# Kernel tuning notes

Measured on AMD Instinct MI355X. Metric: run time of the kernel, lower is better.

The kernel has to match this reference:

```python
import jax, jax.numpy as jnp
import numpy as np
from jax import lax

E, D, I, K = 8, 1024, 2048, 2
B, S = 4, 1024


def setup_inputs() -> dict:
    key = jax.random.key(0)
    k1, k2, k3, k4, k5 = jax.random.split(key, 5)
    x = jax.random.normal(k1, (B, S, D), dtype=jnp.float32)
    routing_weights = jax.random.uniform(k2, (B, S, K), dtype=jnp.float32)
    selected_experts = jax.random.randint(k3, (B, S, K), 0, E).astype(jnp.int64)
    w1 = 0.02 * jax.random.normal(k4, (E, D, I), dtype=jnp.float32)
    w2 = 0.02 * jax.random.normal(k5, (E, I, D), dtype=jnp.float32)
    return {"x": x, "routing_weights": routing_weights,
            "selected_experts": selected_experts, "w1": w1, "w2": w2}


def reference(x, routing_weights, selected_experts, w1, w2):
    shape = x.shape
    d = shape[-1]
    xf = x.reshape(-1, d)                       # [T, D]
    rw = routing_weights.reshape(xf.shape[0], -1)   # [T, K]
    se = selected_experts.reshape(xf.shape[0], -1)  # [T, K]
    n_experts = w1.shape[0]

    def body(acc, inputs):
        e, w1e, w2e = inputs
        # per-token combine weight for expert e (rw assumed >= 0; zero weight == not routed)
        wt = jnp.sum(jnp.where(se == e, rw, 0.0), axis=-1)  # [T]
        h = jax.nn.silu(xf @ w1e)                # [T, I]
        out = h @ w2e                            # [T, D]
        return acc + out * wt[:, None], None

    acc0 = jnp.zeros_like(xf)
    acc, _ = lax.scan(body, acc0, (jnp.arange(n_experts), w1, w2))
    return acc.reshape(shape)
```

## Files before the change

kernel.cpp:

```cpp
#include <hip/hip_runtime.h>
#include <stdint.h>

#define E_EXPERTS 8
#define D_DIM 1024
#define I_DIM 2048
#define T_TOKENS 4096
#define NSLOTS 8192
#define TILE 128
#define MAXPAD (NSLOTS + E_EXPERTS * TILE)
#define TPX 9

#define XCVT_BLOCKS 2048
#define PREP_GRID (1 + XCVT_BLOCKS + 4096)

typedef __attribute__((ext_vector_type(8))) short bf16x8;
typedef __attribute__((ext_vector_type(4))) float f32x4;

__device__ __forceinline__ unsigned short f2b(float f) {
  union { float f; uint32_t u; } v; v.f = f;
  uint32_t r = v.u + 0x7FFFu + ((v.u >> 16) & 1u);
  return (unsigned short)(r >> 16);
}
__device__ __forceinline__ float b2f(unsigned short u) {
  union { uint32_t u; float f; } v; v.u = ((uint32_t)u) << 16; return v.f;
}

__device__ __forceinline__ void async16(const unsigned short* g, unsigned short* l) {
  __builtin_amdgcn_global_load_lds(
      (const __attribute__((address_space(1))) void*)g,
      (__attribute__((address_space(3))) void*)l, 16, 0, 0);
}

__global__ __launch_bounds__(256) void prep_k(
    const float* __restrict__ x, const float* __restrict__ w1, const float* __restrict__ w2,
    const int* __restrict__ se,
    unsigned short* __restrict__ xb, unsigned short* __restrict__ w1t,
    unsigned short* __restrict__ w2t,
    int* __restrict__ ntiles, int* __restrict__ desc,
    int* __restrict__ tok, int* __restrict__ slot_of) {
  int b = blockIdx.x;
  int tid = threadIdx.x;

  if (b == 0) {
    __shared__ int scnt[E_EXPERTS], sbase[E_EXPERTS + 1], scur[E_EXPERTS];
    if (tid < E_EXPERTS) scnt[tid] = 0;
    __syncthreads();
    for (int s = tid; s < NSLOTS; s += 256) atomicAdd(&scnt[se[s]], 1);
    __syncthreads();
    if (tid == 0) {
      int acc = 0, nt = 0;
      for (int e = 0; e < E_EXPERTS; e++) {
        int n = scnt[e];
        sbase[e] = acc;
        scur[e] = acc;
        int pad = (n + TILE - 1) & ~(TILE - 1);
        for (int m = 0; m * TILE < pad; m++) { desc[2 * nt] = e; desc[2 * nt + 1] = acc + m * TILE; nt++; }
        acc += pad;
      }
      sbase[E_EXPERTS] = acc;
      *ntiles = nt;
    }
    __syncthreads();
    for (int e = 0; e < E_EXPERTS; e++) {
      int s0 = sbase[e] + scnt[e], s1 = sbase[e + 1];
      for (int s = s0 + tid; s < s1; s += 256) tok[s] = 0;
    }
    for (int s = tid; s < NSLOTS; s += 256) {
      int e = se[s];
      int pos = atomicAdd(&scur[e], 1);
      tok[pos] = s >> 1;
      slot_of[s] = pos;
    }
    return;
  }

  int bb = b - 1;

  if (bb < XCVT_BLOCKS) {
    size_t i = ((size_t)bb * 256 + tid) * 8;
    float4 v0 = *(const float4*)(x + i);
    float4 v1 = *(const float4*)(x + i + 4);
    ushort4 o0, o1;
    o0.x = f2b(v0.x); o0.y = f2b(v0.y); o0.z = f2b(v0.z); o0.w = f2b(v0.w);
    o1.x = f2b(v1.x); o1.y = f2b(v1.y); o1.z = f2b(v1.z); o1.w = f2b(v1.w);
    *(ushort4*)(xb + i) = o0;
    *(ushort4*)(xb + i + 4) = o1;
    return;
  }

  __shared__ float ts[64 * 129];
  int wb = bb - XCVT_BLOCKS;
  int mat = wb >> 11;
  int sub = wb & 2047;
  int e = sub >> 8, rem = sub & 255;
  const float* src; unsigned short* dst; int C, k0, n0;
  if (mat == 0) {
    int nt = rem >> 4, kt = rem & 15;
    C = I_DIM; k0 = kt * 64; n0 = nt * 128;
    src = w1 + (size_t)e * D_DIM * I_DIM;
    dst = w1t + ((size_t)((e * 16 + nt) * 16 + kt)) * 8192;
  } else {
    int nt = rem >> 5, kt = rem & 31;
    C = D_DIM; k0 = kt * 64; n0 = nt * 128;
    src = w2 + (size_t)e * D_DIM * I_DIM;
    dst = w2t + ((size_t)((e * 8 + nt) * 32 + kt)) * 8192;
  }

  int lrow = tid & 7, c4 = (tid >> 3) * 4;
#pragma unroll
  for (int i = 0; i < 8; i++) {
    int row = i * 8 + lrow;
    float4 v = *(const float4*)(src + (size_t)(k0 + row) * C + n0 + c4);
    float* d = ts + row * 129 + c4;
    d[0] = v.x; d[1] = v.y; d[2] = v.z; d[3] = v.w;
  }
  __syncthreads();
#pragma unroll
  for (int j = 0; j < 4; j++) {
    int q = j * 256 + tid;
    int rr = q >> 3, cc8 = q & 7;
    int c = cc8 ^ (rr & 7);
    bf16x8 o;
#pragma unroll
    for (int t = 0; t < 8; t++)
      o[t] = (short)f2b(ts[(c * 8 + t) * 129 + rr]);
    *(bf16x8*)(dst + (size_t)q * 8) = o;
  }
}

template <int KLEN, int KFULL, int NDIM, int PHASE>
__global__ __launch_bounds__(256) void moe_gemm_k(
    const unsigned short* __restrict__ Amat, const unsigned short* __restrict__ Bt,
    const int* __restrict__ desc, const int* __restrict__ ntiles_p,
    const int* __restrict__ tok, unsigned short* __restrict__ Hout) {
  int id = blockIdx.x;
  int xcd = id & 7, r = id >> 3;
  int ti = xcd * TPX + r % TPX;
  int q = r / TPX;
  int nb, kh;
  if (PHASE == 1) { nb = q; kh = 0; }
  else           { kh = q & 1; nb = q >> 1; }
  if (ti >= *ntiles_p) return;
  int e = desc[2 * ti];
  int slot0 = desc[2 * ti + 1];

  __shared__ unsigned short As[128 * 64];
  __shared__ unsigned short Bs[128 * 64];

  int tid = threadIdx.x;
  int lane = tid & 63;
  int wave = tid >> 6;
  int wm = (wave >> 1) * 64, wn = (wave & 1) * 64;
  int l15 = lane & 15, quad = lane >> 4;

  f32x4 acc[4][4] = {};

  int sr = tid >> 3;
  int ldoff = (((lane & 7) ^ (lane >> 3)) * 8);

  const unsigned short* arow[4];
#pragma unroll
  for (int p = 0; p < 4; p++) {
    int rr = sr + p * 32;
    int row = (PHASE == 1) ? tok[slot0 + rr] : (slot0 + rr);
    arow[p] = Amat + (size_t)row * KFULL + kh * KLEN + ldoff;
  }
  const unsigned short* Bpack =
      Bt + ((((size_t)e * (NDIM / 128) + nb) * (KFULL / 64) + (size_t)kh * (KLEN / 64)) << 13) +
      (size_t)tid * 8;

  for (int kt = 0; kt < KLEN / 64; kt++) {
    int k0 = kt * 64;
#pragma unroll
    for (int p = 0; p < 4; p++) {
      unsigned short* adst = As + (size_t)(p * 256 + wave * 64) * 8;
      unsigned short* bdst = Bs + (size_t)(p * 256 + wave * 64) * 8;
      async16(arow[p] + k0, adst);
      async16(Bpack + (size_t)kt * 8192 + p * 2048, bdst);
    }
    __syncthreads();
#pragma unroll
    for (int ks = 0; ks < 2; ks++) {
      bf16x8 af[4], bfr[4];
#pragma unroll
      for (int i = 0; i < 4; i++) {
        int rr = wm + i * 16 + l15;
        int cc = (((ks * 4 + quad) ^ (rr & 7)) * 8);
        af[i] = *(const bf16x8*)&As[rr * 64 + cc];
      }
#pragma unroll
      for (int j = 0; j < 4; j++) {
        int rr = wn + j * 16 + l15;
        int cc = (((ks * 4 + quad) ^ (rr & 7)) * 8);
        bfr[j] = *(const bf16x8*)&Bs[rr * 64 + cc];
      }
#pragma unroll
      for (int i = 0; i < 4; i++)
#pragma unroll
        for (int j = 0; j < 4; j++)
          acc[i][j] = __builtin_amdgcn_mfma_f32_16x16x32_bf16(bfr[j], af[i], acc[i][j], 0, 0, 0);
    }
    __syncthreads();
  }

#pragma unroll
  for (int i = 0; i < 4; i++) {
    int slotr = slot0 + wm + i * 16 + l15;
    size_t base = (PHASE == 1) ? (size_t)slotr * NDIM
                               : ((size_t)kh * MAXPAD + slotr) * NDIM;
#pragma unroll
    for (int j = 0; j < 4; j++) {
      int colbase = nb * 128 + wn + j * 16 + quad * 4;
      ushort4 o;
#pragma unroll
      for (int rg = 0; rg < 4; rg++) {
        float v = acc[i][j][rg];
        if (PHASE == 1) v = v / (1.f + __expf(-v));
        ((unsigned short*)&o)[rg] = f2b(v);
      }
      *(ushort4*)(Hout + base + colbase) = o;
    }
  }
}

__global__ void combine_k(const unsigned short* __restrict__ y, const float* __restrict__ rw,
                          const int* __restrict__ slot_of, float* __restrict__ out) {
  int g = blockIdx.x * blockDim.x + threadIdx.x;
  int t = g >> 7, dd = (g & 127) * 8;
  int s0 = slot_of[2 * t], s1 = slot_of[2 * t + 1];
  float w0 = rw[2 * t], w1 = rw[2 * t + 1];
  bf16x8 a = *(const bf16x8*)(y + (size_t)s0 * D_DIM + dd);
  bf16x8 bq = *(const bf16x8*)(y + ((size_t)MAXPAD + s0) * D_DIM + dd);
  bf16x8 c = *(const bf16x8*)(y + (size_t)s1 * D_DIM + dd);
  bf16x8 d = *(const bf16x8*)(y + ((size_t)MAXPAD + s1) * D_DIM + dd);
  float4 o0, o1;
  float* o = (float*)&o0;
#pragma unroll
  for (int k = 0; k < 8; k++) {
    float v = w0 * (b2f((unsigned short)a[k]) + b2f((unsigned short)bq[k])) +
              w1 * (b2f((unsigned short)c[k]) + b2f((unsigned short)d[k]));
    if (k < 4) ((float*)&o0)[k] = v; else ((float*)&o1)[k - 4] = v;
  }
  (void)o;
  float* op = out + (size_t)t * D_DIM + dd;
  *(float4*)op = o0;
  *(float4*)(op + 4) = o1;
}

extern "C" void kernel_launch(void* const* d_in, const int* in_sizes, int n_in,
                              void* d_out, int out_size, void* d_ws, size_t ws_size,
                              hipStream_t stream) {
  (void)in_sizes; (void)n_in; (void)ws_size; (void)out_size;
  const float* x  = (const float*)d_in[0];
  const float* rw = (const float*)d_in[1];
  const int*   se = (const int*)d_in[2];
  const float* w1 = (const float*)d_in[3];
  const float* w2 = (const float*)d_in[4];
  float* out = (float*)d_out;
  char* ws = (char*)d_ws;

  int* ntiles  = (int*)(ws + 128);
  int* desc    = (int*)(ws + 256);
  int* tok     = (int*)(ws + 4096);
  int* slot_of = (int*)(ws + 40960);
  unsigned short* xb   = (unsigned short*)(ws + 131072);
  unsigned short* w1t  = xb + (size_t)T_TOKENS * D_DIM;
  unsigned short* w2t  = w1t + (size_t)E_EXPERTS * D_DIM * I_DIM;
  unsigned short* hbuf = w2t + (size_t)E_EXPERTS * D_DIM * I_DIM;
  unsigned short* ypart = xb;

  prep_k<<<PREP_GRID, 256, 0, stream>>>(x, w1, w2, se, xb, w1t, w2t,
                                        ntiles, desc, tok, slot_of);
  moe_gemm_k<1024, 1024, I_DIM, 1><<<8 * TPX * (I_DIM / 128), 256, 0, stream>>>(
      xb, w1t, desc, ntiles, tok, hbuf);
  moe_gemm_k<1024, 2048, D_DIM, 2><<<8 * TPX * (D_DIM / 128) * 2, 256, 0, stream>>>(
      hbuf, w2t, desc, ntiles, tok, ypart);

  combine_k<<<T_TOKENS * 128 / 256, 256, 0, stream>>>(ypart, rw, slot_of, out);
}
```

Baseline: 299.0 us.

## Overlap w2 weight packing with first expert GEMM in a fused launch

The w2 fp32-to-bf16 transpose packing moves out of the prep kernel and into the first GEMM kernel as extra leading blocks, so it runs alongside the phase-1 GEMM instead of before it. This is meant to hide the w2 packing memory traffic behind GEMM1 compute and shorten the prep kernel. The fused kernel uses a shared LDS buffer sized for the transpose tile, which may lower GEMM occupancy. The GEMM and pack bodies are factored into device functions.

```diff
diff --git a/kernel.cpp b/kernel.cpp
--- a/kernel.cpp
+++ b/kernel.cpp
@@ -11,7 +11,10 @@
 #define TPX 9
 
 #define XCVT_BLOCKS 2048
-#define PREP_GRID (1 + XCVT_BLOCKS + 4096)
+#define WPACK_BLOCKS 2048
+#define PREP_GRID (1 + XCVT_BLOCKS + WPACK_BLOCKS)
+#define G1_GEMM_BLOCKS (8 * TPX * (I_DIM / 128))
+#define G1_GRID (WPACK_BLOCKS + G1_GEMM_BLOCKS)
 
 typedef __attribute__((ext_vector_type(8))) short bf16x8;
 typedef __attribute__((ext_vector_type(4))) float f32x4;
@@ -29,6 +32,137 @@
   __builtin_amdgcn_global_load_lds(
       (const __attribute__((address_space(1))) void*)g,
       (__attribute__((address_space(3))) void*)l, 16, 0, 0);
+}
+
+__device__ __forceinline__ void wpack_body(
+    int mat, int sub, float* ts, int tid,
+    const float* __restrict__ w1, const float* __restrict__ w2,
+    unsigned short* __restrict__ w1t, unsigned short* __restrict__ w2t) {
+  int e = sub >> 8, rem = sub & 255;
+  const float* src; unsigned short* dst; int C, k0, n0;
+  if (mat == 0) {
+    int nt = rem >> 4, kt = rem & 15;
+    C = I_DIM; k0 = kt * 64; n0 = nt * 128;
+    src = w1 + (size_t)e * D_DIM * I_DIM;
+    dst = w1t + ((size_t)((e * 16 + nt) * 16 + kt)) * 8192;
+  } else {
+    int nt = rem >> 5, kt = rem & 31;
+    C = D_DIM; k0 = kt * 64; n0 = nt * 128;
+    src = w2 + (size_t)e * D_DIM * I_DIM;
+    dst = w2t + ((size_t)((e * 8 + nt) * 32 + kt)) * 8192;
+  }
+  int lrow = tid & 7, c4 = (tid >> 3) * 4;
+#pragma unroll
+  for (int i = 0; i < 8; i++) {
+    int row = i * 8 + lrow;
+    float4 v = *(const float4*)(src + (size_t)(k0 + row) * C + n0 + c4);
+    float* d = ts + row * 129 + c4;
+    d[0] = v.x; d[1] = v.y; d[2] = v.z; d[3] = v.w;
+  }
+  __syncthreads();
+#pragma unroll
+  for (int j = 0; j < 4; j++) {
+    int q = j * 256 + tid;
+    int rr = q >> 3, cc8 = q & 7;
+    int c = cc8 ^ (rr & 7);
+    bf16x8 o;
+#pragma unroll
+    for (int t = 0; t < 8; t++)
+      o[t] = (short)f2b(ts[(c * 8 + t) * 129 + rr]);
+    *(bf16x8*)(dst + (size_t)q * 8) = o;
+  }
+}
+
+template <int KLEN, int KFULL, int NDIM, int PHASE>
+__device__ __forceinline__ void moe_gemm_body(
+    int id, unsigned short* As, unsigned short* Bs,
+    const unsigned short* __restrict__ Amat, const unsigned short* __restrict__ Bt,
+    const int* __restrict__ desc, const int* __restrict__ ntiles_p,
+    const int* __restrict__ tok, unsigned short* __restrict__ Hout) {
+  int xcd = id & 7, r = id >> 3;
+  int ti = xcd * TPX + r % TPX;
+  int q = r / TPX;
+  int nb, kh;
+  if (PHASE == 1) { nb = q; kh = 0; }
+  else           { kh = q & 1; nb = q >> 1; }
+  if (ti >= *ntiles_p) return;
+  int e = desc[2 * ti];
+  int slot0 = desc[2 * ti + 1];
+
+  int tid = threadIdx.x;
+  int lane = tid & 63;
+  int wave = tid >> 6;
+  int wm = (wave >> 1) * 64, wn = (wave & 1) * 64;
+  int l15 = lane & 15, quad = lane >> 4;
+
+  f32x4 acc[4][4] = {};
+
+  int sr = tid >> 3;
+  int ldoff = (((lane & 7) ^ (lane >> 3)) * 8);
+
+  const unsigned short* arow[4];
+#pragma unroll
+  for (int p = 0; p < 4; p++) {
+    int rr = sr + p * 32;
+    int row = (PHASE == 1) ? tok[slot0 + rr] : (slot0 + rr);
+    arow[p] = Amat + (size_t)row * KFULL + kh * KLEN + ldoff;
+  }
+  const unsigned short* Bpack =
+      Bt + ((((size_t)e * (NDIM / 128) + nb) * (KFULL / 64) + (size_t)kh * (KLEN / 64)) << 13) +
+      (size_t)tid * 8;
+
+  for (int kt = 0; kt < KLEN / 64; kt++) {
+    int k0 = kt * 64;
+#pragma unroll
+    for (int p = 0; p < 4; p++) {
+      unsigned short* adst = As + (size_t)(p * 256 + wave * 64) * 8;
+      unsigned short* bdst = Bs + (size_t)(p * 256 + wave * 64) * 8;
+      async16(arow[p] + k0, adst);
+      async16(Bpack + (size_t)kt * 8192 + p * 2048, bdst);
+    }
+    __syncthreads();
+#pragma unroll
+    for (int ks = 0; ks < 2; ks++) {
+      bf16x8 af[4], bfr[4];
+#pragma unroll
+      for (int i = 0; i < 4; i++) {
+        int rr = wm + i * 16 + l15;
+        int cc = (((ks * 4 + quad) ^ (rr & 7)) * 8);
+        af[i] = *(const bf16x8*)&As[rr * 64 + cc];
+      }
+#pragma unroll
+      for (int j = 0; j < 4; j++) {
+        int rr = wn + j * 16 + l15;
+        int cc = (((ks * 4 + quad) ^ (rr & 7)) * 8);
+        bfr[j] = *(const bf16x8*)&Bs[rr * 64 + cc];
+      }
+#pragma unroll
+      for (int i = 0; i < 4; i++)
+#pragma unroll
+        for (int j = 0; j < 4; j++)
+          acc[i][j] = __builtin_amdgcn_mfma_f32_16x16x32_bf16(bfr[j], af[i], acc[i][j], 0, 0, 0);
+    }
+    __syncthreads();
+  }
+
+#pragma unroll
+  for (int i = 0; i < 4; i++) {
+    int slotr = slot0 + wm + i * 16 + l15;
+    size_t base = (PHASE == 1) ? (size_t)slotr * NDIM
+                               : ((size_t)kh * MAXPAD + slotr) * NDIM;
+#pragma unroll
+    for (int j = 0; j < 4; j++) {
+      int colbase = nb * 128 + wn + j * 16 + quad * 4;
+      ushort4 o;
+#pragma unroll
+      for (int rg = 0; rg < 4; rg++) {
+        float v = acc[i][j][rg];
+        if (PHASE == 1) v = v / (1.f + __expf(-v));
+        ((unsigned short*)&o)[rg] = f2b(v);
+      }
+      *(ushort4*)(Hout + base + colbase) = o;
+    }
+  }
 }
 
 __global__ __launch_bounds__(256) void prep_k(
@@ -89,138 +223,36 @@
   }
 
   __shared__ float ts[64 * 129];
-  int wb = bb - XCVT_BLOCKS;
-  int mat = wb >> 11;
-  int sub = wb & 2047;
-  int e = sub >> 8, rem = sub & 255;
-  const float* src; unsigned short* dst; int C, k0, n0;
-  if (mat == 0) {
-    int nt = rem >> 4, kt = rem & 15;
-    C = I_DIM; k0 = kt * 64; n0 = nt * 128;
-    src = w1 + (size_t)e * D_DIM * I_DIM;
-    dst = w1t + ((size_t)((e * 16 + nt) * 16 + kt)) * 8192;
-  } else {
-    int nt = rem >> 5, kt = rem & 31;
-    C = D_DIM; k0 = kt * 64; n0 = nt * 128;
-    src = w2 + (size_t)e * D_DIM * I_DIM;
-    dst = w2t + ((size_t)((e * 8 + nt) * 32 + kt)) * 8192;
-  }
-
-  int lrow = tid & 7, c4 = (tid >> 3) * 4;
-#pragma unroll
-  for (int i = 0; i < 8; i++) {
-    int row = i * 8 + lrow;
-    float4 v = *(const float4*)(src + (size_t)(k0 + row) * C + n0 + c4);
-    float* d = ts + row * 129 + c4;
-    d[0] = v.x; d[1] = v.y; d[2] = v.z; d[3] = v.w;
-  }
-  __syncthreads();
-#pragma unroll
-  for (int j = 0; j < 4; j++) {
-    int q = j * 256 + tid;
-    int rr = q >> 3, cc8 = q & 7;
-    int c = cc8 ^ (rr & 7);
-    bf16x8 o;
-#pragma unroll
-    for (int t = 0; t < 8; t++)
-      o[t] = (short)f2b(ts[(c * 8 + t) * 129 + rr]);
-    *(bf16x8*)(dst + (size_t)q * 8) = o;
-  }
-}
-
-template <int KLEN, int KFULL, int NDIM, int PHASE>
-__global__ __launch_bounds__(256) void moe_gemm_k(
+  wpack_body(0, bb - XCVT_BLOCKS, ts, tid, w1, w2, w1t, w2t);
+}
+
+__global__ __launch_bounds__(256) void g1_fused_k(
+    const float* __restrict__ w1, const float* __restrict__ w2,
+    unsigned short* __restrict__ w1t, unsigned short* __restrict__ w2t,
+    const unsigned short* __restrict__ xb,
+    const int* __restrict__ desc, const int* __restrict__ ntiles_p,
+    const int* __restrict__ tok, unsigned short* __restrict__ hbuf) {
+  __shared__ __align__(16) char smem[64 * 129 * 4];
+  int b = blockIdx.x;
+  int tid = threadIdx.x;
+  if (b < WPACK_BLOCKS) {
+    wpack_body(1, b, (float*)smem, tid, w1, w2, w1t, w2t);
+    return;
+  }
+  unsigned short* As = (unsigned short*)smem;
+  unsigned short* Bs = As + 8192;
+  moe_gemm_body<1024, 1024, I_DIM, 1>(b - WPACK_BLOCKS, As, Bs,
+                                      xb, w1t, desc, ntiles_p, tok, hbuf);
+}
+
+__global__ __launch_bounds__(256) void gemm2_k(
     const unsigned short* __restrict__ Amat, const unsigned short* __restrict__ Bt,
     const int* __restrict__ desc, const int* __restrict__ ntiles_p,
     const int* __restrict__ tok, unsigned short* __restrict__ Hout) {
-  int id = blockIdx.x;
-  int xcd = id & 7, r = id >> 3;
-  int ti = xcd * TPX + r % TPX;
-  int q = r / TPX;
-  int nb, kh;
-  if (PHASE == 1) { nb = q; kh = 0; }
-  else           { kh = q & 1; nb = q >> 1; }
-  if (ti >= *ntiles_p) return;
-  int e = desc[2 * ti];
-  int slot0 = desc[2 * ti + 1];
-
   __shared__ unsigned short As[128 * 64];
   __shared__ unsigned short Bs[128 * 64];
-
-  int tid = threadIdx.x;
-  int lane = tid & 63;
-  int wave = tid >> 6;
-  int wm = (wave >> 1) * 64, wn = (wave & 1) * 64;
-  int l15 = lane & 15, quad = lane >> 4;
-
-  f32x4 acc[4][4] = {};
-
-  int sr = tid >> 3;
-  int ldoff = (((lane & 7) ^ (lane >> 3)) * 8);
-
-  const unsigned short* arow[4];
-#pragma unroll
-  for (int p = 0; p < 4; p++) {
-    int rr = sr + p * 32;
-    int row = (PHASE == 1) ? tok[slot0 + rr] : (slot0 + rr);
-    arow[p] = Amat + (size_t)row * KFULL + kh * KLEN + ldoff;
-  }
-  const unsigned short* Bpack =
-      Bt + ((((size_t)e * (NDIM / 128) + nb) * (KFULL / 64) + (size_t)kh * (KLEN / 64)) << 13) +
-      (size_t)tid * 8;
-
-  for (int kt = 0; kt < KLEN / 64; kt++) {
-    int k0 = kt * 64;
-#pragma unroll
-    for (int p = 0; p < 4; p++) {
-      unsigned short* adst = As + (size_t)(p * 256 + wave * 64) * 8;
-      unsigned short* bdst = Bs + (size_t)(p * 256 + wave * 64) * 8;
-      async16(arow[p] + k0, adst);
-      async16(Bpack + (size_t)kt * 8192 + p * 2048, bdst);
-    }
-    __syncthreads();
-#pragma unroll
-    for (int ks = 0; ks < 2; ks++) {
-      bf16x8 af[4], bfr[4];
-#pragma unroll
-      for (int i = 0; i < 4; i++) {
-        int rr = wm + i * 16 + l15;
-        int cc = (((ks * 4 + quad) ^ (rr & 7)) * 8);
-        af[i] = *(const bf16x8*)&As[rr * 64 + cc];
-      }
-#pragma unroll
-      for (int j = 0; j < 4; j++) {
-        int rr = wn + j * 16 + l15;
-        int cc = (((ks * 4 + quad) ^ (rr & 7)) * 8);
-        bfr[j] = *(const bf16x8*)&Bs[rr * 64 + cc];
-      }
-#pragma unroll
-      for (int i = 0; i < 4; i++)
-#pragma unroll
-        for (int j = 0; j < 4; j++)
-          acc[i][j] = __builtin_amdgcn_mfma_f32_16x16x32_bf16(bfr[j], af[i], acc[i][j], 0, 0, 0);
-    }
-    __syncthreads();
-  }
-
-#pragma unroll
-  for (int i = 0; i < 4; i++) {
-    int slotr = slot0 + wm + i * 16 + l15;
-    size_t base = (PHASE == 1) ? (size_t)slotr * NDIM
-                               : ((size_t)kh * MAXPAD + slotr) * NDIM;
-#pragma unroll
-    for (int j = 0; j < 4; j++) {
-      int colbase = nb * 128 + wn + j * 16 + quad * 4;
-      ushort4 o;
-#pragma unroll
-      for (int rg = 0; rg < 4; rg++) {
-        float v = acc[i][j][rg];
-        if (PHASE == 1) v = v / (1.f + __expf(-v));
-        ((unsigned short*)&o)[rg] = f2b(v);
-      }
-      *(ushort4*)(Hout + base + colbase) = o;
-    }
-  }
+  moe_gemm_body<1024, 2048, D_DIM, 2>(blockIdx.x, As, Bs,
+                                      Amat, Bt, desc, ntiles_p, tok, Hout);
 }
 
 __global__ void combine_k(const unsigned short* __restrict__ y, const float* __restrict__ rw,
@@ -234,14 +266,12 @@
   bf16x8 c = *(const bf16x8*)(y + (size_t)s1 * D_DIM + dd);
   bf16x8 d = *(const bf16x8*)(y + ((size_t)MAXPAD + s1) * D_DIM + dd);
   float4 o0, o1;
-  float* o = (float*)&o0;
 #pragma unroll
   for (int k = 0; k < 8; k++) {
     float v = w0 * (b2f((unsigned short)a[k]) + b2f((unsigned short)bq[k])) +
               w1 * (b2f((unsigned short)c[k]) + b2f((unsigned short)d[k]));
     if (k < 4) ((float*)&o0)[k] = v; else ((float*)&o1)[k - 4] = v;
   }
-  (void)o;
   float* op = out + (size_t)t * D_DIM + dd;
   *(float4*)op = o0;
   *(float4*)(op + 4) = o1;
@@ -271,9 +301,9 @@
 
   prep_k<<<PREP_GRID, 256, 0, stream>>>(x, w1, w2, se, xb, w1t, w2t,
                                         ntiles, desc, tok, slot_of);
-  moe_gemm_k<1024, 1024, I_DIM, 1><<<8 * TPX * (I_DIM / 128), 256, 0, stream>>>(
-      xb, w1t, desc, ntiles, tok, hbuf);
-  moe_gemm_k<1024, 2048, D_DIM, 2><<<8 * TPX * (D_DIM / 128) * 2, 256, 0, stream>>>(
+  g1_fused_k<<<G1_GRID, 256, 0, stream>>>(w1, w2, w1t, w2t,
+                                          xb, desc, ntiles, tok, hbuf);
+  gemm2_k<<<8 * TPX * (D_DIM / 128) * 2, 256, 0, stream>>>(
       hbuf, w2t, desc, ntiles, tok, ypart);
 
   combine_k<<<T_TOKENS * 128 / 256, 256, 0, stream>>>(ypart, rw, slot_of, out);
```

New measurement: 309.7 us. 1.04x slower.

## Fuse weight bf16 conversion into GEMM tile loads, drop weight prepass

Applied to the files above, without the earlier changes.

Removes the prep pass that transposed and converted w1/w2 from fp32 to bf16 into a packed workspace layout. Each GEMM block now loads fp32 weight rows directly, converts them to bf16 in registers, and writes them swizzled into LDS, while A tiles stay on async LDS loads. This aims to remove a large full-weight read/write pass and its extra launch work. The trade-off is that fp32 weights are re-read by every token tile through L2/MALL, and the B loads become synchronous register loads that may stall the main loop.

```diff
diff --git a/kernel.cpp b/kernel.cpp
--- a/kernel.cpp
+++ b/kernel.cpp
@@ -11,7 +11,7 @@
 #define TPX 9
 
 #define XCVT_BLOCKS 2048
-#define PREP_GRID (1 + XCVT_BLOCKS + 4096)
+#define PREP_GRID (1 + XCVT_BLOCKS)
 
 typedef __attribute__((ext_vector_type(8))) short bf16x8;
 typedef __attribute__((ext_vector_type(4))) float f32x4;
@@ -32,10 +32,8 @@
 }
 
 __global__ __launch_bounds__(256) void prep_k(
-    const float* __restrict__ x, const float* __restrict__ w1, const float* __restrict__ w2,
-    const int* __restrict__ se,
-    unsigned short* __restrict__ xb, unsigned short* __restrict__ w1t,
-    unsigned short* __restrict__ w2t,
+    const float* __restrict__ x, const int* __restrict__ se,
+    unsigned short* __restrict__ xb,
     int* __restrict__ ntiles, int* __restrict__ desc,
     int* __restrict__ tok, int* __restrict__ slot_of) {
   int b = blockIdx.x;
@@ -75,62 +73,19 @@
   }
 
   int bb = b - 1;
-
-  if (bb < XCVT_BLOCKS) {
-    size_t i = ((size_t)bb * 256 + tid) * 8;
-    float4 v0 = *(const float4*)(x + i);
-    float4 v1 = *(const float4*)(x + i + 4);
-    ushort4 o0, o1;
-    o0.x = f2b(v0.x); o0.y = f2b(v0.y); o0.z = f2b(v0.z); o0.w = f2b(v0.w);
-    o1.x = f2b(v1.x); o1.y = f2b(v1.y); o1.z = f2b(v1.z); o1.w = f2b(v1.w);
-    *(ushort4*)(xb + i) = o0;
-    *(ushort4*)(xb + i + 4) = o1;
-    return;
-  }
-
-  __shared__ float ts[64 * 129];
-  int wb = bb - XCVT_BLOCKS;
-  int mat = wb >> 11;
-  int sub = wb & 2047;
-  int e = sub >> 8, rem = sub & 255;
-  const float* src; unsigned short* dst; int C, k0, n0;
-  if (mat == 0) {
-    int nt = rem >> 4, kt = rem & 15;
-    C = I_DIM; k0 = kt * 64; n0 = nt * 128;
-    src = w1 + (size_t)e * D_DIM * I_DIM;
-    dst = w1t + ((size_t)((e * 16 + nt) * 16 + kt)) * 8192;
-  } else {
-    int nt = rem >> 5, kt = rem & 31;
-    C = D_DIM; k0 = kt * 64; n0 = nt * 128;
-    src = w2 + (size_t)e * D_DIM * I_DIM;
-    dst = w2t + ((size_t)((e * 8 + nt) * 32 + kt)) * 8192;
-  }
-
-  int lrow = tid & 7, c4 = (tid >> 3) * 4;
-#pragma unroll
-  for (int i = 0; i < 8; i++) {
-    int row = i * 8 + lrow;
-    float4 v = *(const float4*)(src + (size_t)(k0 + row) * C + n0 + c4);
-    float* d = ts + row * 129 + c4;
-    d[0] = v.x; d[1] = v.y; d[2] = v.z; d[3] = v.w;
-  }
-  __syncthreads();
-#pragma unroll
-  for (int j = 0; j < 4; j++) {
-    int q = j * 256 + tid;
-    int rr = q >> 3, cc8 = q & 7;
-    int c = cc8 ^ (rr & 7);
-    bf16x8 o;
-#pragma unroll
-    for (int t = 0; t < 8; t++)
-      o[t] = (short)f2b(ts[(c * 8 + t) * 129 + rr]);
-    *(bf16x8*)(dst + (size_t)q * 8) = o;
-  }
+  size_t i = ((size_t)bb * 256 + tid) * 8;
+  float4 v0 = *(const float4*)(x + i);
+  float4 v1 = *(const float4*)(x + i + 4);
+  ushort4 o0, o1;
+  o0.x = f2b(v0.x); o0.y = f2b(v0.y); o0.z = f2b(v0.z); o0.w = f2b(v0.w);
+  o1.x = f2b(v1.x); o1.y = f2b(v1.y); o1.z = f2b(v1.z); o1.w = f2b(v1.w);
+  *(ushort4*)(xb + i) = o0;
+  *(ushort4*)(xb + i + 4) = o1;
 }
 
 template <int KLEN, int KFULL, int NDIM, int PHASE>
 __global__ __launch_bounds__(256) void moe_gemm_k(
-    const unsigned short* __restrict__ Amat, const unsigned short* __restrict__ Bt,
+    const unsigned short* __restrict__ Amat, const float* __restrict__ Wf,
     const int* __restrict__ desc, const int* __restrict__ ntiles_p,
     const int* __restrict__ tok, unsigned short* __restrict__ Hout) {
   int id = blockIdx.x;
@@ -155,8 +110,8 @@
 
   f32x4 acc[4][4] = {};
 
+  int ldoff = (((lane & 7) ^ (lane >> 3)) * 8);
   int sr = tid >> 3;
-  int ldoff = (((lane & 7) ^ (lane >> 3)) * 8);
 
   const unsigned short* arow[4];
 #pragma unroll
@@ -165,18 +120,33 @@
     int row = (PHASE == 1) ? tok[slot0 + rr] : (slot0 + rr);
     arow[p] = Amat + (size_t)row * KFULL + kh * KLEN + ldoff;
   }
-  const unsigned short* Bpack =
-      Bt + ((((size_t)e * (NDIM / 128) + nb) * (KFULL / 64) + (size_t)kh * (KLEN / 64)) << 13) +
-      (size_t)tid * 8;
+
+  int u = tid & 7, m = tid >> 3;
+  const float* bsrc = Wf + (size_t)e * D_DIM * I_DIM +
+                      (size_t)(kh * KLEN + u * 8) * NDIM + nb * 128 + m * 4;
+  unsigned short* bdst[4];
+#pragma unroll
+  for (int j = 0; j < 4; j++) {
+    int n = m * 4 + j;
+    bdst[j] = &Bs[n * 64 + (u ^ (n & 7)) * 8];
+  }
 
   for (int kt = 0; kt < KLEN / 64; kt++) {
     int k0 = kt * 64;
-#pragma unroll
-    for (int p = 0; p < 4; p++) {
-      unsigned short* adst = As + (size_t)(p * 256 + wave * 64) * 8;
-      unsigned short* bdst = Bs + (size_t)(p * 256 + wave * 64) * 8;
-      async16(arow[p] + k0, adst);
-      async16(Bpack + (size_t)kt * 8192 + p * 2048, bdst);
+    float4 f[8];
+#pragma unroll
+    for (int rr8 = 0; rr8 < 8; rr8++)
+      f[rr8] = *(const float4*)(bsrc + (size_t)(k0 + rr8) * NDIM);
+#pragma unroll
+    for (int p = 0; p < 4; p++)
+      async16(arow[p] + k0, As + (size_t)(p * 256 + wave * 64) * 8);
+#pragma unroll
+    for (int j = 0; j < 4; j++) {
+      bf16x8 o;
+#pragma unroll
+      for (int t = 0; t < 8; t++)
+        o[t] = (short)f2b(((const float*)&f[t])[j]);
+      *(bf16x8*)bdst[j] = o;
     }
     __syncthreads();
 #pragma unroll
@@ -234,14 +204,12 @@
   bf16x8 c = *(const bf16x8*)(y + (size_t)s1 * D_DIM + dd);
   bf16x8 d = *(const bf16x8*)(y + ((size_t)MAXPAD + s1) * D_DIM + dd);
   float4 o0, o1;
-  float* o = (float*)&o0;
 #pragma unroll
   for (int k = 0; k < 8; k++) {
     float v = w0 * (b2f((unsigned short)a[k]) + b2f((unsigned short)bq[k])) +
               w1 * (b2f((unsigned short)c[k]) + b2f((unsigned short)d[k]));
     if (k < 4) ((float*)&o0)[k] = v; else ((float*)&o1)[k - 4] = v;
   }
-  (void)o;
   float* op = out + (size_t)t * D_DIM + dd;
   *(float4*)op = o0;
   *(float4*)(op + 4) = o1;
@@ -264,17 +232,14 @@
   int* tok     = (int*)(ws + 4096);
   int* slot_of = (int*)(ws + 40960);
   unsigned short* xb   = (unsigned short*)(ws + 131072);
-  unsigned short* w1t  = xb + (size_t)T_TOKENS * D_DIM;
-  unsigned short* w2t  = w1t + (size_t)E_EXPERTS * D_DIM * I_DIM;
-  unsigned short* hbuf = w2t + (size_t)E_EXPERTS * D_DIM * I_DIM;
-  unsigned short* ypart = xb;
-
-  prep_k<<<PREP_GRID, 256, 0, stream>>>(x, w1, w2, se, xb, w1t, w2t,
-                                        ntiles, desc, tok, slot_of);
+  unsigned short* hbuf = xb + (size_t)T_TOKENS * D_DIM;
+  unsigned short* ypart = hbuf + (size_t)MAXPAD * I_DIM;
+
+  prep_k<<<PREP_GRID, 256, 0, stream>>>(x, se, xb, ntiles, desc, tok, slot_of);
   moe_gemm_k<1024, 1024, I_DIM, 1><<<8 * TPX * (I_DIM / 128), 256, 0, stream>>>(
-      xb, w1t, desc, ntiles, tok, hbuf);
+      xb, w1, desc, ntiles, tok, hbuf);
   moe_gemm_k<1024, 2048, D_DIM, 2><<<8 * TPX * (D_DIM / 128) * 2, 256, 0, stream>>>(
-      hbuf, w2t, desc, ntiles, tok, ypart);
+      hbuf, w2, desc, ntiles, tok, ypart);
 
   combine_k<<<T_TOKENS * 128 / 256, 256, 0, stream>>>(ypart, rw, slot_of, out);
 }
```

After: 411.3 us. 1.38x slower.

## Double-buffer LDS tiles to overlap async global loads with MFMA compute

Applied to the files above, without the earlier changes.

The MoE GEMM main loop now uses two LDS buffers for the A and B tiles and issues the async loads for the next K-tile before computing on the current one. It waits with s_waitcnt vmcnt(8) so only the previous stage's loads must have landed, and raises wave priority around the MFMA block. The aim is to hide global-memory latency behind compute instead of stalling on a full barrier every iteration. In exchange LDS use doubles to 64KB per block, which may lower occupancy.

```diff
diff --git a/kernel.cpp b/kernel.cpp
--- a/kernel.cpp
+++ b/kernel.cpp
@@ -144,8 +144,8 @@
   int e = desc[2 * ti];
   int slot0 = desc[2 * ti + 1];
 
-  __shared__ unsigned short As[128 * 64];
-  __shared__ unsigned short Bs[128 * 64];
+  __shared__ unsigned short As[2][128 * 64];
+  __shared__ unsigned short Bs[2][128 * 64];
 
   int tid = threadIdx.x;
   int lane = tid & 63;
@@ -169,16 +169,15 @@
       Bt + ((((size_t)e * (NDIM / 128) + nb) * (KFULL / 64) + (size_t)kh * (KLEN / 64)) << 13) +
       (size_t)tid * 8;
 
-  for (int kt = 0; kt < KLEN / 64; kt++) {
-    int k0 = kt * 64;
+  auto stage = [&](int t, unsigned short* Ad, unsigned short* Bd) {
+    int k0 = t * 64;
 #pragma unroll
     for (int p = 0; p < 4; p++) {
-      unsigned short* adst = As + (size_t)(p * 256 + wave * 64) * 8;
-      unsigned short* bdst = Bs + (size_t)(p * 256 + wave * 64) * 8;
-      async16(arow[p] + k0, adst);
-      async16(Bpack + (size_t)kt * 8192 + p * 2048, bdst);
-    }
-    __syncthreads();
+      async16(arow[p] + k0, Ad + (size_t)(p * 256 + wave * 64) * 8);
+      async16(Bpack + (size_t)t * 8192 + p * 2048, Bd + (size_t)(p * 256 + wave * 64) * 8);
+    }
+  };
+  auto compute = [&](const unsigned short* Ac, const unsigned short* Bc) {
 #pragma unroll
     for (int ks = 0; ks < 2; ks++) {
       bf16x8 af[4], bfr[4];
@@ -186,13 +185,13 @@
       for (int i = 0; i < 4; i++) {
         int rr = wm + i * 16 + l15;
         int cc = (((ks * 4 + quad) ^ (rr & 7)) * 8);
-        af[i] = *(const bf16x8*)&As[rr * 64 + cc];
+        af[i] = *(const bf16x8*)&Ac[rr * 64 + cc];
       }
 #pragma unroll
       for (int j = 0; j < 4; j++) {
         int rr = wn + j * 16 + l15;
         int cc = (((ks * 4 + quad) ^ (rr & 7)) * 8);
-        bfr[j] = *(const bf16x8*)&Bs[rr * 64 + cc];
+        bfr[j] = *(const bf16x8*)&Bc[rr * 64 + cc];
       }
 #pragma unroll
       for (int i = 0; i < 4; i++)
@@ -200,8 +199,27 @@
         for (int j = 0; j < 4; j++)
           acc[i][j] = __builtin_amdgcn_mfma_f32_16x16x32_bf16(bfr[j], af[i], acc[i][j], 0, 0, 0);
     }
-    __syncthreads();
-  }
+  };
+
+  constexpr int NT = KLEN / 64;
+  stage(0, As[0], Bs[0]);
+  for (int t = 0; t < NT - 1; ++t) {
+    unsigned short* Ac = As[t & 1];
+    unsigned short* Bc = Bs[t & 1];
+    stage(t + 1, As[(t + 1) & 1], Bs[(t + 1) & 1]);
+    asm volatile("s_waitcnt vmcnt(8)" ::: "memory");
+    __builtin_amdgcn_s_barrier();
+    __builtin_amdgcn_sched_barrier(0);
+    __builtin_amdgcn_s_setprio(1);
+    compute(Ac, Bc);
+    __builtin_amdgcn_s_setprio(0);
+    __builtin_amdgcn_sched_barrier(0);
+    __builtin_amdgcn_s_barrier();
+  }
+  asm volatile("s_waitcnt vmcnt(0)" ::: "memory");
+  __builtin_amdgcn_s_barrier();
+  __builtin_amdgcn_sched_barrier(0);
+  compute(As[(NT - 1) & 1], Bs[(NT - 1) & 1]);
 
 #pragma unroll
   for (int i = 0; i < 4; i++) {
@@ -234,14 +252,12 @@
   bf16x8 c = *(const bf16x8*)(y + (size_t)s1 * D_DIM + dd);
   bf16x8 d = *(const bf16x8*)(y + ((size_t)MAXPAD + s1) * D_DIM + dd);
   float4 o0, o1;
-  float* o = (float*)&o0;
 #pragma unroll
   for (int k = 0; k < 8; k++) {
     float v = w0 * (b2f((unsigned short)a[k]) + b2f((unsigned short)bq[k])) +
               w1 * (b2f((unsigned short)c[k]) + b2f((unsigned short)d[k]));
     if (k < 4) ((float*)&o0)[k] = v; else ((float*)&o1)[k - 4] = v;
   }
-  (void)o;
   float* op = out + (size_t)t * D_DIM + dd;
   *(float4*)op = o0;
   *(float4*)(op + 4) = o1;
```

Result: slower. 321.0 us (+7.4%).
